# Kernel optimization log

Measured on AMD Instinct MI355X. Metric: run time of the kernel, lower is better.

## Reference

```python
import jax, jax.numpy as jnp
import numpy as np

TAU = 2.0       # spikingjelly LIFNode default tau
V_TH = 1.0      # default v_threshold
T_STEPS = 16
MAX_ACTION = 1.0
ALPHA = 4.0     # surrogate.Sigmoid default alpha

@jax.custom_vjp
def spike(x):
    # Heaviside(v - v_th) with sigmoid surrogate gradient
    return (x >= 0).astype(x.dtype)

def _spike_fwd(x):
    return spike(x), x

def _spike_bwd(x, g):
    s = jax.nn.sigmoid(ALPHA * x)
    return (g * ALPHA * s * (1.0 - s),)

spike.defvjp(_spike_fwd, _spike_bwd)

def setup_inputs() -> dict:
    key = jax.random.key(0)
    ks = jax.random.split(key, 7)
    B, S, H, A = 131072, 128, 256, 8
    def lin(k, out_d, in_d):
        return jax.random.normal(k, (out_d, in_d), jnp.float32) / np.sqrt(in_d)
    return {
        "state": jax.random.normal(ks[0], (B, S), jnp.float32),
        "W1": lin(ks[1], H, S),
        "b1": jax.random.normal(ks[2], (H,), jnp.float32) * 0.1,
        "W2": lin(ks[3], H, H),
        "b2": jax.random.normal(ks[4], (H,), jnp.float32) * 0.1,
        "W3": lin(ks[5], A, H),
        "b3": jax.random.normal(ks[6], (A,), jnp.float32) * 0.1,
    }

def reference(state, W1, b1, W2, b2, W3, b3):
    B = state.shape[0]
    H, A = W1.shape[0], W3.shape[0]
    # input current to layer 1 is identical every step -> hoist out of scan
    h1 = state @ W1.T + b1  # [B, 256]
    v0 = (jnp.zeros((B, H), state.dtype),
          jnp.zeros((B, H), state.dtype),
          jnp.zeros((B, A), state.dtype))

    def step(carry, _):
        v1, v2, v3 = carry
        # LIF 1: decay_input charge, hard reset to v_reset=0
        v1 = v1 + (h1 - v1) / TAU
        s1 = spike(v1 - V_TH)
        v1 = v1 * (1.0 - s1)
        # LIF 2
        h2 = s1 @ W2.T + b2
        v2 = v2 + (h2 - v2) / TAU
        s2 = spike(v2 - V_TH)
        v2 = v2 * (1.0 - s2)
        # NonSpiking LIF: charge only, no spike/reset
        h3 = s2 @ W3.T + b3
        v3 = v3 + (h3 - v3) / TAU
        return (v1, v2, v3), None

    (v1, v2, v3), _ = jax.lax.scan(step, v0, None, length=T_STEPS)
    return MAX_ACTION * jnp.tanh(v3)
```

## Files before the change

### kernel.cpp

```cpp
#include <hip/hip_runtime.h>
#include <hip/hip_bf16.h>
#include <math.h>

#define S_DIM 128
#define H_DIM 256
#define A_DIM 8
#define T_STEPS 16
#define BT 8
#define EPS_BAND 2e-4f
#define TS 18

typedef __attribute__((ext_vector_type(8))) short short8;
typedef __attribute__((ext_vector_type(8))) unsigned short ushort8;
typedef __attribute__((ext_vector_type(4))) float f32x4;

__device__ inline unsigned short f32_to_bf16_rn(float f) {
    unsigned int u = __float_as_uint(f);
    return (unsigned short)((u + 0x7FFFu + ((u >> 16) & 1u)) >> 16);
}
__device__ inline float bf16_bits_to_f32(unsigned short b) {
    return __uint_as_float(((unsigned int)b) << 16);
}

__device__ __forceinline__ void make_pat(
    const float* __restrict__ state, const float* __restrict__ W1,
    double b1d, int n1, int bh, long bset, unsigned short* __restrict__ patdst)
{
    double acc[4] = {0.0, 0.0, 0.0, 0.0};
    const float4* w1p = reinterpret_cast<const float4*>(W1 + n1 * S_DIM);
    const float4* sp  = reinterpret_cast<const float4*>(state + (bset * BT + bh * 4) * S_DIM);
    #pragma unroll 4
    for (int kq = 0; kq < 32; ++kq) {
        const float4 w4 = w1p[kq];
        const double wd0 = (double)w4.x, wd1 = (double)w4.y;
        const double wd2 = (double)w4.z, wd3 = (double)w4.w;
        #pragma unroll
        for (int b4 = 0; b4 < 4; ++b4) {
            const float4 s4 = sp[b4 * 32 + kq];
            double a = acc[b4];
            a = fma(wd0, (double)s4.x, a);
            a = fma(wd1, (double)s4.y, a);
            a = fma(wd2, (double)s4.z, a);
            a = fma(wd3, (double)s4.w, a);
            acc[b4] = a;
        }
    }
    #pragma unroll
    for (int b4 = 0; b4 < 4; ++b4) {
        const double h1 = acc[b4] + b1d;
        double v = 0.0;
        unsigned int p = 0;
        #pragma unroll
        for (int t = 0; t < T_STEPS; ++t) {
            v = v + (h1 - v) * 0.5;
            if (v >= 1.0) { p |= (1u << t); v = 0.0; }
        }
        patdst[(bh * 4 + b4) * 256 + n1] = (unsigned short)p;
    }
}

__global__ __launch_bounds__(512, 2)
void snn_pers(const float* __restrict__ state,
              const float* __restrict__ W1, const float* __restrict__ b1,
              const float* __restrict__ W2, const float* __restrict__ b2,
              const float* __restrict__ W3, const float* __restrict__ b3,
              float* __restrict__ out,
              unsigned int* __restrict__ gcount, unsigned int* __restrict__ glist,
              unsigned int listcap, int nIter)
{
    __shared__ unsigned short atile[8 * 4096];
    __shared__ unsigned short pat[2][8 * 256];
    __shared__ float tbuf[8][64 * TS];
    __shared__ float st_u[8 * 260];
    __shared__ float w3s[A_DIM * 260];
    __shared__ float red3[8][64];
    __shared__ unsigned int flagw;

    const int tid = threadIdx.x;
    const int l = tid & 63, w = tid >> 6;
    const int cl = l & 15, c8 = l >> 4;

    if (tid == 0) flagw = 0;

    {
        const int a = tid >> 6, c = tid & 63;
        const float4 v = reinterpret_cast<const float4*>(W3)[tid];
        *reinterpret_cast<float4*>(&w3s[a * 260 + c * 4]) = v;
    }

    short8 bhi[2][8], bmid[2][8];
    #pragma unroll
    for (int nt = 0; nt < 2; ++nt) {
        const int n = w * 32 + nt * 16 + cl;
        #pragma unroll
        for (int ks = 0; ks < 8; ++ks) {
            const float* src = W2 + n * H_DIM + ks * 32 + c8 * 8;
            const float4 a0 = *reinterpret_cast<const float4*>(src);
            const float4 a1 = *reinterpret_cast<const float4*>(src + 4);
            const float wv[8] = {a0.x, a0.y, a0.z, a0.w, a1.x, a1.y, a1.z, a1.w};
            short8 hi8, mi8;
            #pragma unroll
            for (int e = 0; e < 8; ++e) {
                const unsigned short hb = f32_to_bf16_rn(wv[e]);
                const float rem = wv[e] - bf16_bits_to_f32(hb);
                hi8[e] = (short)hb;
                mi8[e] = (short)f32_to_bf16_rn(rem);
            }
            bhi[nt][ks] = hi8;
            bmid[nt][ks] = mi8;
        }
    }
    const float b2r = b2[w * 32 + (l & 31)];
    const int n1 = tid & 255, bh = tid >> 8;
    const double b1d = (double)b1[n1];

    const long bsetBase = (long)blockIdx.x * nIter;

    make_pat(state, W1, b1d, n1, bh, bsetBase, &pat[0][0]);
    __syncthreads();

    #pragma unroll 1
    for (int it = 0; it < nIter; ++it) {
        const int cur = it & 1;
        const long b0 = (bsetBase + it) * BT;

        {
            const int jb = w * 32 + c8 * 8;
            #pragma unroll
            for (int b = 0; b < 8; ++b) {
                const ushort8 p8 = *reinterpret_cast<const ushort8*>(&pat[cur][b * 256 + jb]);
                short8 af;
                #pragma unroll
                for (int e = 0; e < 8; ++e)
                    af[e] = (short)((((unsigned int)p8[e] >> cl) & 1u) ? 0x3F80 : 0);
                *reinterpret_cast<short8*>(&atile[b * 4096 + tid * 8]) = af;
            }
        }
        __syncthreads();

        #pragma unroll 1
        for (int p2 = 0; p2 < 4; ++p2) {
            f32x4 c0 = {0,0,0,0}, c1 = {0,0,0,0}, c2 = {0,0,0,0}, c3 = {0,0,0,0};
            f32x4 c4 = {0,0,0,0}, c5 = {0,0,0,0}, c6 = {0,0,0,0}, c7 = {0,0,0,0};
            #pragma unroll
            for (int ks = 0; ks < 8; ++ks) {
                const short8 af0 = *reinterpret_cast<const short8*>(
                    &atile[(2 * p2) * 4096 + (ks * 64 + l) * 8]);
                const short8 af1 = *reinterpret_cast<const short8*>(
                    &atile[(2 * p2 + 1) * 4096 + (ks * 64 + l) * 8]);
                c0 = __builtin_amdgcn_mfma_f32_16x16x32_bf16(af0, bhi[0][ks],  c0, 0, 0, 0);
                c1 = __builtin_amdgcn_mfma_f32_16x16x32_bf16(af0, bmid[0][ks], c1, 0, 0, 0);
                c2 = __builtin_amdgcn_mfma_f32_16x16x32_bf16(af0, bhi[1][ks],  c2, 0, 0, 0);
                c3 = __builtin_amdgcn_mfma_f32_16x16x32_bf16(af0, bmid[1][ks], c3, 0, 0, 0);
                c4 = __builtin_amdgcn_mfma_f32_16x16x32_bf16(af1, bhi[0][ks],  c4, 0, 0, 0);
                c5 = __builtin_amdgcn_mfma_f32_16x16x32_bf16(af1, bmid[0][ks], c5, 0, 0, 0);
                c6 = __builtin_amdgcn_mfma_f32_16x16x32_bf16(af1, bhi[1][ks],  c6, 0, 0, 0);
                c7 = __builtin_amdgcn_mfma_f32_16x16x32_bf16(af1, bmid[1][ks], c7, 0, 0, 0);
            }
            const f32x4 a00 = c0 + c1, a01 = c2 + c3, a10 = c4 + c5, a11 = c6 + c7;

            float* tb = &tbuf[w][0];
            const int col = 4 * c8;
            *reinterpret_cast<float2*>(&tb[cl * TS + col])            = make_float2(a00[0], a00[1]);
            *reinterpret_cast<float2*>(&tb[cl * TS + col + 2])        = make_float2(a00[2], a00[3]);
            *reinterpret_cast<float2*>(&tb[(16 + cl) * TS + col])     = make_float2(a01[0], a01[1]);
            *reinterpret_cast<float2*>(&tb[(16 + cl) * TS + col + 2]) = make_float2(a01[2], a01[3]);
            *reinterpret_cast<float2*>(&tb[(32 + cl) * TS + col])     = make_float2(a10[0], a10[1]);
            *reinterpret_cast<float2*>(&tb[(32 + cl) * TS + col + 2]) = make_float2(a10[2], a10[3]);
            *reinterpret_cast<float2*>(&tb[(48 + cl) * TS + col])     = make_float2(a11[0], a11[1]);
            *reinterpret_cast<float2*>(&tb[(48 + cl) * TS + col + 2]) = make_float2(a11[2], a11[3]);

            {
                const int rm = l & 31, rbb = l >> 5;
                const float* tr = &tbuf[w][(rbb * 32 + rm) * TS];
                float v2 = 0.0f, vmin = 1e9f;
                unsigned int m = 0;
                #pragma unroll
                for (int g = 0; g < 8; ++g) {
                    const float2 h2 = *reinterpret_cast<const float2*>(&tr[g * 2]);
                    {
                        const float v = (v2 + (h2.x + b2r)) * 0.5f;
                        vmin = fminf(vmin, fabsf(v - 1.0f));
                        const bool sp = v >= 1.0f;
                        v2 = sp ? 0.0f : v;
                        m |= sp ? (1u << (2 * g)) : 0u;
                    }
                    {
                        const float v = (v2 + (h2.y + b2r)) * 0.5f;
                        vmin = fminf(vmin, fabsf(v - 1.0f));
                        const bool sp = v >= 1.0f;
                        v2 = sp ? 0.0f : v;
                        m |= sp ? (1u << (2 * g + 1)) : 0u;
                    }
                }
                const int b = 2 * p2 + rbb;
                st_u[b * 260 + w * 32 + rm] = (float)m * 0x1p-16f;
                if (vmin < EPS_BAND) atomicOr(&flagw, 1u << b);
            }
        }

        if (it + 1 < nIter)
            make_pat(state, W1, b1d, n1, bh, bsetBase + it + 1, &pat[cur ^ 1][0]);

        __syncthreads();

        const unsigned int flcopy = (tid < BT) ? flagw : 0u;

        {
            const int task = tid & 63, chunk = tid >> 6;
            const int b = task >> 3, a = task & 7;
            const int j0 = chunk * 32;
            float s0 = 0, s1v = 0, s2v = 0, s3 = 0;
            #pragma unroll
            for (int qq = 0; qq < 8; ++qq) {
                const float4 uv = *reinterpret_cast<const float4*>(&st_u[b * 260 + j0 + qq * 4]);
                const float4 wv = *reinterpret_cast<const float4*>(&w3s[a * 260 + j0 + qq * 4]);
                s0 = fmaf(uv.x, wv.x, s0);
                s1v = fmaf(uv.y, wv.y, s1v);
                s2v = fmaf(uv.z, wv.z, s2v);
                s3 = fmaf(uv.w, wv.w, s3);
            }
            red3[chunk][task] = (s0 + s1v) + (s2v + s3);
        }
        __syncthreads();

        if (tid < 64) {
            const int a = tid & 7;
            const float h = ((red3[0][tid] + red3[1][tid]) + (red3[2][tid] + red3[3][tid]))
                          + ((red3[4][tid] + red3[5][tid]) + (red3[6][tid] + red3[7][tid]))
                          + b3[a] * (1.0f - 0x1p-16f);
            out[b0 * A_DIM + tid] = tanhf(h);
        }
        if (tid < BT && ((flcopy >> tid) & 1u)) {
            const unsigned int idx = atomicAdd(gcount, 1u);
            if (idx < listcap) glist[idx] = (unsigned int)(b0 + tid);
        }
        if (tid == 0) flagw = 0;
    }
}

__global__ __launch_bounds__(512, 2)
void snn_fix(const float* __restrict__ state,
             const float* __restrict__ W1, const float* __restrict__ b1,
             const float* __restrict__ W2, const float* __restrict__ b2,
             const float* __restrict__ W3, const float* __restrict__ b3,
             float* __restrict__ out,
             const unsigned int* __restrict__ gcount,
             const unsigned int* __restrict__ glist,
             unsigned int listcap)
{
    __shared__ float  s1s[H_DIM];
    __shared__ double redh[H_DIM];
    __shared__ double uu[H_DIM];

    const int tid = threadIdx.x;
    const int n = tid & 255;
    const int kh = tid >> 8;
    unsigned int cnt = *gcount;
    if (cnt > listcap) cnt = listcap;
    if (cnt == 0) return;

    float4 w2f[32];
    #pragma unroll
    for (int q = 0; q < 32; ++q)
        w2f[q] = reinterpret_cast<const float4*>(W2 + n * H_DIM + kh * 128)[q];

    const double b1d = (double)b1[n];
    const double b2d = (double)b2[n];

    for (unsigned int i = blockIdx.x; i < cnt; i += gridDim.x) {
        const long be = (long)glist[i];

        double hp = 0.0;
        {
            const float* w1p = W1 + n * S_DIM + kh * 64;
            const float* stp = state + be * S_DIM + kh * 64;
            #pragma unroll
            for (int kq = 0; kq < 16; ++kq) {
                const float4 w4 = reinterpret_cast<const float4*>(w1p)[kq];
                const float4 s4 = reinterpret_cast<const float4*>(stp)[kq];
                hp = fma((double)w4.x, (double)s4.x, hp);
                hp = fma((double)w4.y, (double)s4.y, hp);
                hp = fma((double)w4.z, (double)s4.z, hp);
                hp = fma((double)w4.w, (double)s4.w, hp);
            }
        }
        if (kh) redh[n] = hp;
        __syncthreads();
        double h1 = 0.0, v1 = 0.0, v2 = 0.0, un = 0.0;
        if (!kh) h1 = hp + redh[n] + b1d;
        double ct = 0x1p-16;

        for (int t = 0; t < T_STEPS; ++t) {
            if (!kh) {
                v1 = v1 + (h1 - v1) * 0.5;
                const bool sp = (v1 >= 1.0);
                v1 = sp ? 0.0 : v1;
                s1s[n] = sp ? 1.0f : 0.0f;
            }
            __syncthreads();
            double h2p = 0.0;
            #pragma unroll
            for (int q = 0; q < 32; ++q) {
                const float4 w4 = w2f[q];
                const float4 s4 = *reinterpret_cast<const float4*>(&s1s[kh * 128 + q * 4]);
                h2p = fma((double)w4.x, (double)s4.x, h2p);
                h2p = fma((double)w4.y, (double)s4.y, h2p);
                h2p = fma((double)w4.z, (double)s4.z, h2p);
                h2p = fma((double)w4.w, (double)s4.w, h2p);
            }
            __syncthreads();
            if (kh) redh[n] = h2p;
            __syncthreads();
            if (!kh) {
                const double h2 = h2p + redh[n] + b2d;
                v2 = v2 + (h2 - v2) * 0.5;
                const bool sp = (v2 >= 1.0);
                v2 = sp ? 0.0 : v2;
                un += sp ? ct : 0.0;
            }
            ct *= 2.0;
        }
        if (!kh) uu[n] = un;
        __syncthreads();
        if (tid < A_DIM) {
            double d0 = 0, d1 = 0, d2 = 0, d3 = 0;
            const float* w3p = W3 + tid * H_DIM;
            for (int j = 0; j < H_DIM; j += 4) {
                d0 = fma((double)w3p[j],     uu[j],     d0);
                d1 = fma((double)w3p[j + 1], uu[j + 1], d1);
                d2 = fma((double)w3p[j + 2], uu[j + 2], d2);
                d3 = fma((double)w3p[j + 3], uu[j + 3], d3);
            }
            const double v3 = (d0 + d1) + (d2 + d3) + (double)b3[tid] * (1.0 - 0x1p-16);
            out[be * A_DIM + tid] = (float)tanh(v3);
        }
        __syncthreads();
    }
}

extern "C" void kernel_launch(void* const* d_in, const int* in_sizes, int n_in,
                              void* d_out, int out_size, void* d_ws, size_t ws_size,
                              hipStream_t stream)
{
    const float* state = (const float*)d_in[0];
    const float* W1    = (const float*)d_in[1];
    const float* b1    = (const float*)d_in[2];
    const float* W2    = (const float*)d_in[3];
    const float* b2    = (const float*)d_in[4];
    const float* W3    = (const float*)d_in[5];
    const float* b3    = (const float*)d_in[6];
    float* out = (float*)d_out;

    unsigned int* gcount = (unsigned int*)d_ws;
    unsigned int* glist  = (unsigned int*)d_ws + 4;
    const unsigned int listcap =
        (ws_size > 64) ? (unsigned int)((ws_size - 16) / 4) : 0;

    hipMemsetAsync(d_ws, 0, 16, stream);

    const int B = in_sizes[0] / S_DIM;
    const int GRID = 256;
    const int nIter = B / (GRID * BT);

    snn_pers<<<GRID, 512, 0, stream>>>(state, W1, b1, W2, b2, W3, b3,
                                       out, gcount, glist, listcap, nIter);
    snn_fix<<<2048, 512, 0, stream>>>(state, W1, b1, W2, b2, W3, b3,
                                      out, gcount, glist, listcap);
}
```

Baseline: 1.624 ms.

## Halve batch tile, replace LDS transpose with shuffle scan, raise occupancy

Halves the per-iteration batch tile from 8 to 4 rows. The LIF-2 time recurrence now runs directly on MFMA accumulator fragments through a pipelined cross-lane shuffle scan, which removes the tbuf LDS transpose buffer. The pattern buffer is single-buffered, hi/mid MFMA products share one accumulator, and the grid grows to 1024 blocks with launch bounds allowing 6 blocks per CU, all aimed at cutting LDS use and raising occupancy and latency hiding. The tighter register budget risks spills, the serialized 7-step shuffle scan adds latency, and smaller tiles mean more per-iteration syncs.

Result: slower. 4.471 ms (+175.4%).

```diff
diff --git a/kernel.cpp b/kernel.cpp
--- a/kernel.cpp
+++ b/kernel.cpp
@@ -6,9 +6,8 @@
 #define H_DIM 256
 #define A_DIM 8
 #define T_STEPS 16
-#define BT 8
+#define BT 4
 #define EPS_BAND 2e-4f
-#define TS 18
 
 typedef __attribute__((ext_vector_type(8))) short short8;
 typedef __attribute__((ext_vector_type(8))) unsigned short ushort8;
@@ -22,32 +21,32 @@
     return __uint_as_float(((unsigned int)b) << 16);
 }
 
-__device__ __forceinline__ void make_pat(
+__device__ __forceinline__ void make_pat2(
     const float* __restrict__ state, const float* __restrict__ W1,
     double b1d, int n1, int bh, long bset, unsigned short* __restrict__ patdst)
 {
-    double acc[4] = {0.0, 0.0, 0.0, 0.0};
+    double acc[2] = {0.0, 0.0};
     const float4* w1p = reinterpret_cast<const float4*>(W1 + n1 * S_DIM);
-    const float4* sp  = reinterpret_cast<const float4*>(state + (bset * BT + bh * 4) * S_DIM);
+    const float4* sp  = reinterpret_cast<const float4*>(state + (bset * BT + bh * 2) * S_DIM);
     #pragma unroll 4
     for (int kq = 0; kq < 32; ++kq) {
         const float4 w4 = w1p[kq];
         const double wd0 = (double)w4.x, wd1 = (double)w4.y;
         const double wd2 = (double)w4.z, wd3 = (double)w4.w;
         #pragma unroll
-        for (int b4 = 0; b4 < 4; ++b4) {
-            const float4 s4 = sp[b4 * 32 + kq];
-            double a = acc[b4];
+        for (int b2i = 0; b2i < 2; ++b2i) {
+            const float4 s4 = sp[b2i * 32 + kq];
+            double a = acc[b2i];
             a = fma(wd0, (double)s4.x, a);
             a = fma(wd1, (double)s4.y, a);
             a = fma(wd2, (double)s4.z, a);
             a = fma(wd3, (double)s4.w, a);
-            acc[b4] = a;
+            acc[b2i] = a;
         }
     }
     #pragma unroll
-    for (int b4 = 0; b4 < 4; ++b4) {
-        const double h1 = acc[b4] + b1d;
+    for (int b2i = 0; b2i < 2; ++b2i) {
+        const double h1 = acc[b2i] + b1d;
         double v = 0.0;
         unsigned int p = 0;
         #pragma unroll
@@ -55,11 +54,11 @@
             v = v + (h1 - v) * 0.5;
             if (v >= 1.0) { p |= (1u << t); v = 0.0; }
         }
-        patdst[(bh * 4 + b4) * 256 + n1] = (unsigned short)p;
-    }
-}
-
-__global__ __launch_bounds__(512, 2)
+        patdst[(bh * 2 + b2i) * 256 + n1] = (unsigned short)p;
+    }
+}
+
+__global__ __launch_bounds__(512, 6)
 void snn_pers(const float* __restrict__ state,
               const float* __restrict__ W1, const float* __restrict__ b1,
               const float* __restrict__ W2, const float* __restrict__ b2,
@@ -68,12 +67,11 @@
               unsigned int* __restrict__ gcount, unsigned int* __restrict__ glist,
               unsigned int listcap, int nIter)
 {
-    __shared__ unsigned short atile[8 * 4096];
-    __shared__ unsigned short pat[2][8 * 256];
-    __shared__ float tbuf[8][64 * TS];
-    __shared__ float st_u[8 * 260];
+    __shared__ unsigned short atile[BT * 4096];
+    __shared__ unsigned short pat[BT * 256];
+    __shared__ float st_u[BT * 260];
     __shared__ float w3s[A_DIM * 260];
-    __shared__ float red3[8][64];
+    __shared__ float red3[8][BT * A_DIM];
     __shared__ unsigned int flagw;
 
     const int tid = threadIdx.x;
@@ -110,25 +108,25 @@
             bmid[nt][ks] = mi8;
         }
     }
-    const float b2r = b2[w * 32 + (l & 31)];
+    const float b2lo = b2[w * 32 + cl];
+    const float b2hi = b2[w * 32 + 16 + cl];
     const int n1 = tid & 255, bh = tid >> 8;
     const double b1d = (double)b1[n1];
 
     const long bsetBase = (long)blockIdx.x * nIter;
 
-    make_pat(state, W1, b1d, n1, bh, bsetBase, &pat[0][0]);
+    make_pat2(state, W1, b1d, n1, bh, bsetBase, pat);
     __syncthreads();
 
     #pragma unroll 1
     for (int it = 0; it < nIter; ++it) {
-        const int cur = it & 1;
         const long b0 = (bsetBase + it) * BT;
 
         {
             const int jb = w * 32 + c8 * 8;
             #pragma unroll
-            for (int b = 0; b < 8; ++b) {
-                const ushort8 p8 = *reinterpret_cast<const ushort8*>(&pat[cur][b * 256 + jb]);
+            for (int b = 0; b < BT; ++b) {
+                const ushort8 p8 = *reinterpret_cast<const ushort8*>(&pat[b * 256 + jb]);
                 short8 af;
                 #pragma unroll
                 for (int e = 0; e < 8; ++e)
@@ -139,75 +137,82 @@
         __syncthreads();
 
         #pragma unroll 1
-        for (int p2 = 0; p2 < 4; ++p2) {
-            f32x4 c0 = {0,0,0,0}, c1 = {0,0,0,0}, c2 = {0,0,0,0}, c3 = {0,0,0,0};
-            f32x4 c4 = {0,0,0,0}, c5 = {0,0,0,0}, c6 = {0,0,0,0}, c7 = {0,0,0,0};
+        for (int p2 = 0; p2 < 2; ++p2) {
+            f32x4 c00 = {0,0,0,0}, c01 = {0,0,0,0}, c10 = {0,0,0,0}, c11 = {0,0,0,0};
             #pragma unroll
             for (int ks = 0; ks < 8; ++ks) {
                 const short8 af0 = *reinterpret_cast<const short8*>(
                     &atile[(2 * p2) * 4096 + (ks * 64 + l) * 8]);
                 const short8 af1 = *reinterpret_cast<const short8*>(
                     &atile[(2 * p2 + 1) * 4096 + (ks * 64 + l) * 8]);
-                c0 = __builtin_amdgcn_mfma_f32_16x16x32_bf16(af0, bhi[0][ks],  c0, 0, 0, 0);
-                c1 = __builtin_amdgcn_mfma_f32_16x16x32_bf16(af0, bmid[0][ks], c1, 0, 0, 0);
-                c2 = __builtin_amdgcn_mfma_f32_16x16x32_bf16(af0, bhi[1][ks],  c2, 0, 0, 0);
-                c3 = __builtin_amdgcn_mfma_f32_16x16x32_bf16(af0, bmid[1][ks], c3, 0, 0, 0);
-                c4 = __builtin_amdgcn_mfma_f32_16x16x32_bf16(af1, bhi[0][ks],  c4, 0, 0, 0);
-                c5 = __builtin_amdgcn_mfma_f32_16x16x32_bf16(af1, bmid[0][ks], c5, 0, 0, 0);
-                c6 = __builtin_amdgcn_mfma_f32_16x16x32_bf16(af1, bhi[1][ks],  c6, 0, 0, 0);
-                c7 = __builtin_amdgcn_mfma_f32_16x16x32_bf16(af1, bmid[1][ks], c7, 0, 0, 0);
-            }
-            const f32x4 a00 = c0 + c1, a01 = c2 + c3, a10 = c4 + c5, a11 = c6 + c7;
-
-            float* tb = &tbuf[w][0];
-            const int col = 4 * c8;
-            *reinterpret_cast<float2*>(&tb[cl * TS + col])            = make_float2(a00[0], a00[1]);
-            *reinterpret_cast<float2*>(&tb[cl * TS + col + 2])        = make_float2(a00[2], a00[3]);
-            *reinterpret_cast<float2*>(&tb[(16 + cl) * TS + col])     = make_float2(a01[0], a01[1]);
-            *reinterpret_cast<float2*>(&tb[(16 + cl) * TS + col + 2]) = make_float2(a01[2], a01[3]);
-            *reinterpret_cast<float2*>(&tb[(32 + cl) * TS + col])     = make_float2(a10[0], a10[1]);
-            *reinterpret_cast<float2*>(&tb[(32 + cl) * TS + col + 2]) = make_float2(a10[2], a10[3]);
-            *reinterpret_cast<float2*>(&tb[(48 + cl) * TS + col])     = make_float2(a11[0], a11[1]);
-            *reinterpret_cast<float2*>(&tb[(48 + cl) * TS + col + 2]) = make_float2(a11[2], a11[3]);
+                c00 = __builtin_amdgcn_mfma_f32_16x16x32_bf16(af0, bhi[0][ks],  c00, 0, 0, 0);
+                c00 = __builtin_amdgcn_mfma_f32_16x16x32_bf16(af0, bmid[0][ks], c00, 0, 0, 0);
+                c01 = __builtin_amdgcn_mfma_f32_16x16x32_bf16(af0, bhi[1][ks],  c01, 0, 0, 0);
+                c01 = __builtin_amdgcn_mfma_f32_16x16x32_bf16(af0, bmid[1][ks], c01, 0, 0, 0);
+                c10 = __builtin_amdgcn_mfma_f32_16x16x32_bf16(af1, bhi[0][ks],  c10, 0, 0, 0);
+                c10 = __builtin_amdgcn_mfma_f32_16x16x32_bf16(af1, bmid[0][ks], c10, 0, 0, 0);
+                c11 = __builtin_amdgcn_mfma_f32_16x16x32_bf16(af1, bhi[1][ks],  c11, 0, 0, 0);
+                c11 = __builtin_amdgcn_mfma_f32_16x16x32_bf16(af1, bmid[1][ks], c11, 0, 0, 0);
+            }
 
             {
-                const int rm = l & 31, rbb = l >> 5;
-                const float* tr = &tbuf[w][(rbb * 32 + rm) * TS];
-                float v2 = 0.0f, vmin = 1e9f;
-                unsigned int m = 0;
+                const int q = c8;
+                float pv2 = 0.0f, pvm = 1e9f;
+                unsigned int pm = 0u;
+                unsigned int fm[4];
+                float fvm[4];
                 #pragma unroll
-                for (int g = 0; g < 8; ++g) {
-                    const float2 h2 = *reinterpret_cast<const float2*>(&tr[g * 2]);
-                    {
-                        const float v = (v2 + (h2.x + b2r)) * 0.5f;
-                        vmin = fminf(vmin, fabsf(v - 1.0f));
+                for (int s = 0; s < 7; ++s) {
+                    float rv2, rvm;
+                    unsigned int rm;
+                    if (s == 0) { rv2 = 0.0f; rm = 0u; rvm = 1e9f; }
+                    else {
+                        rv2 = __shfl_up(pv2, 16, 64);
+                        rm  = __shfl_up(pm, 16, 64);
+                        rvm = __shfl_up(pvm, 16, 64);
+                        if (q == 0) { rv2 = 0.0f; rm = 0u; rvm = 1e9f; }
+                    }
+                    const int f = s - q;
+                    const int fc = (f < 0) ? 0 : (f > 3 ? 3 : f);
+                    const f32x4 av = (fc == 0) ? c00 : (fc == 1) ? c01
+                                   : (fc == 2) ? c10 : c11;
+                    const float b2f = ((fc & 1) != 0) ? b2hi : b2lo;
+                    float v2 = rv2, vm = rvm;
+                    unsigned int m = rm;
+                    #pragma unroll
+                    for (int r = 0; r < 4; ++r) {
+                        const float v = (v2 + (av[r] + b2f)) * 0.5f;
+                        vm = fminf(vm, fabsf(v - 1.0f));
                         const bool sp = v >= 1.0f;
                         v2 = sp ? 0.0f : v;
-                        m |= sp ? (1u << (2 * g)) : 0u;
+                        m |= (sp ? 1u : 0u) << (4 * q + r);
                     }
-                    {
-                        const float v = (v2 + (h2.y + b2r)) * 0.5f;
-                        vmin = fminf(vmin, fabsf(v - 1.0f));
-                        const bool sp = v >= 1.0f;
-                        v2 = sp ? 0.0f : v;
-                        m |= sp ? (1u << (2 * g + 1)) : 0u;
+                    pv2 = v2; pm = m; pvm = vm;
+                    if (s >= 3) {
+                        if (q == 3) { fm[s - 3] = m; fvm[s - 3] = vm; }
                     }
                 }
-                const int b = 2 * p2 + rbb;
-                st_u[b * 260 + w * 32 + rm] = (float)m * 0x1p-16f;
-                if (vmin < EPS_BAND) atomicOr(&flagw, 1u << b);
+                if (q == 3) {
+                    #pragma unroll
+                    for (int f = 0; f < 4; ++f) {
+                        const int b = 2 * p2 + (f >> 1);
+                        const int n = w * 32 + (f & 1) * 16 + cl;
+                        st_u[b * 260 + n] = (float)fm[f] * 0x1p-16f;
+                        if (fvm[f] < EPS_BAND) atomicOr(&flagw, 1u << b);
+                    }
+                }
             }
         }
 
         if (it + 1 < nIter)
-            make_pat(state, W1, b1d, n1, bh, bsetBase + it + 1, &pat[cur ^ 1][0]);
+            make_pat2(state, W1, b1d, n1, bh, bsetBase + it + 1, pat);
 
         __syncthreads();
 
         const unsigned int flcopy = (tid < BT) ? flagw : 0u;
 
-        {
-            const int task = tid & 63, chunk = tid >> 6;
+        if (tid < 256) {
+            const int task = tid & 31, chunk = tid >> 5;
             const int b = task >> 3, a = task & 7;
             const int j0 = chunk * 32;
             float s0 = 0, s1v = 0, s2v = 0, s3 = 0;
@@ -224,7 +229,7 @@
         }
         __syncthreads();
 
-        if (tid < 64) {
+        if (tid < BT * A_DIM) {
             const int a = tid & 7;
             const float h = ((red3[0][tid] + red3[1][tid]) + (red3[2][tid] + red3[3][tid]))
                           + ((red3[4][tid] + red3[5][tid]) + (red3[6][tid] + red3[7][tid]))
@@ -360,7 +365,7 @@
     hipMemsetAsync(d_ws, 0, 16, stream);
 
     const int B = in_sizes[0] / S_DIM;
-    const int GRID = 256;
+    const int GRID = 1024;
     const int nIter = B / (GRID * BT);
 
     snn_pers<<<GRID, 512, 0, stream>>>(state, W1, b1, W2, b2, W3, b3,
```
